# Kernel optimization log

Hardware: AMD Instinct MI355X
Metric: run time of the kernel (lower is better)

Reference implementation:

```python
import jax, jax.numpy as jnp
import numpy as np

B_, L_, D_, R_, N_ = 8, 1024, 512, 32, 16  # batch, seq(in_channels), dim(=dim_inner), dt_rank, d_state


def setup_inputs() -> dict:
    key = jax.random.key(0)
    ks = jax.random.split(key, 8)
    s = lambda k, shape, scale: jax.random.normal(k, shape, dtype=jnp.float32) * scale
    inv = D_ ** -0.5
    return {
        "x": jax.random.uniform(ks[0], (B_, L_, D_), dtype=jnp.float32),
        "W1": s(ks[1], (D_, D_), inv), "b1": jnp.zeros((D_,), jnp.float32),
        "W2": s(ks[2], (D_, D_), inv), "b2": jnp.zeros((D_,), jnp.float32),
        "Wout": s(ks[3], (D_, D_), inv), "bout": jnp.zeros((D_,), jnp.float32),
        "conv_w": s(ks[4], (L_, L_, 3), (3 * L_) ** -0.5),  # Conv1d(L_, L_, k=3) weight (O,I,W)
        "conv_b": jnp.zeros((L_,), jnp.float32),
        "W_dbc": s(ks[5], (R_ + 2 * N_, D_), inv),          # deltaBC projection (no bias)
        "W_dt": s(ks[6], (D_, R_), R_ ** -0.5),             # dt_proj weight
        "b_dt": jnp.zeros((D_,), jnp.float32),
        "A_log": jnp.log(jnp.tile(jnp.arange(1, N_ + 1, dtype=jnp.float32), (D_, 1))),  # (D, N)
        "Dp": jnp.ones((D_,), jnp.float32),
    }


def _silu(v):
    return v * jax.nn.sigmoid(v)


def _selective_scan(u, delta, A, Bm, Cm, Dp):
    # u, delta: (b, l, d); A: (d, n); Bm, Cm: (b, l, n); Dp: (d,)
    dA = jnp.exp(jnp.einsum('bld,dn->bldn', delta, A))          # (b,l,d,n)
    dBu = jnp.einsum('bld,bln,bld->bldn', delta, Bm, u)          # (b,l,d,n)

    def step(h, inp):
        dA_t, dBu_t, C_t = inp                                   # (b,d,n),(b,d,n),(b,n)
        h = dA_t * h + dBu_t
        return h, jnp.einsum('bdn,bn->bd', h, C_t)

    h0 = jnp.zeros((u.shape[0], u.shape[2], A.shape[1]), u.dtype)
    _, ys = jax.lax.scan(step, h0, (dA.transpose(1, 0, 2, 3), dBu.transpose(1, 0, 2, 3), Cm.transpose(1, 0, 2)))
    return ys.transpose(1, 0, 2) + u * Dp                        # (b,l,d)


def reference(x, W1, b1, W2, b2, Wout, bout, conv_w, conv_b, W_dbc, W_dt, b_dt, A_log, Dp):
    skip = x
    x1 = x @ W1.T + b1                                            # proj_one
    x2 = x @ W2.T + b2                                            # proj_two
    # Conv1d over channel axis = L_ (dim 1), spatial axis = D_ (dim 2)
    x1 = jax.lax.conv_general_dilated(x1, conv_w, window_strides=(1,), padding=((1, 1),),
                                      dimension_numbers=('NCW', 'OIW', 'NCW')) + conv_b[None, :, None]
    x1 = _silu(x1)
    # SSM (zeta-style): deltaBC -> split -> dt_proj -> softplus -> selective scan
    dbc = x1 @ W_dbc.T                                            # (b,l,R+2N)
    delta = jax.nn.softplus(dbc[..., :R_] @ W_dt.T + b_dt)        # (b,l,d)
    Bm, Cm = dbc[..., R_:R_ + N_], dbc[..., R_ + N_:]
    A = -jnp.exp(A_log)
    y = _selective_scan(x1, delta, A, Bm, Cm, Dp)
    out = y * _silu(x2) + skip
    return out @ Wout.T + bout
```

## Files before the change

kernel.cpp:

```cpp
#include <hip/hip_runtime.h>
#include <hip/hip_bf16.h>

typedef __hip_bfloat16 bf16;
typedef __bf16 bf16x8 __attribute__((ext_vector_type(8)));
typedef float f32x4 __attribute__((ext_vector_type(4)));

static_assert(sizeof(bf16) == 2, "bf16 must be 2 bytes");

#define NC 32
#define CH 32
#define X1TP_BSTRIDE (514L * 1024)

__device__ __forceinline__ float silu_f(float v) { return v / (1.0f + __expf(-v)); }

__device__ __forceinline__ void gload16(const bf16* g, bf16* l) {
  __builtin_amdgcn_global_load_lds((const __attribute__((address_space(1))) void*)g,
                                   (__attribute__((address_space(3))) void*)l,
                                   16, 0, 0);
}

template <int N> __device__ __forceinline__ void wait_vm() {
  static_assert(N == 0 || N == 4 || N == 6 || N == 8 || N == 12, "add case");
  if constexpr (N == 0)       asm volatile("s_waitcnt vmcnt(0)" ::: "memory");
  else if constexpr (N == 4)  asm volatile("s_waitcnt vmcnt(4)" ::: "memory");
  else if constexpr (N == 6)  asm volatile("s_waitcnt vmcnt(6)" ::: "memory");
  else if constexpr (N == 8)  asm volatile("s_waitcnt vmcnt(8)" ::: "memory");
  else if constexpr (N == 12) asm volatile("s_waitcnt vmcnt(12)" ::: "memory");
}

__global__ __launch_bounds__(256) void prep_all(
    const float* __restrict__ x, const float* __restrict__ W1,
    const float* __restrict__ W2, const float* __restrict__ Wout,
    const float* __restrict__ Wdbc, const float* __restrict__ convw,
    bf16* __restrict__ xb, bf16* __restrict__ w1b, bf16* __restrict__ w2b,
    bf16* __restrict__ woutb, bf16* __restrict__ wdbcb,
    bf16* __restrict__ cws, bf16* __restrict__ x1tp) {
  const int gid = blockIdx.x * 256 + threadIdx.x;
  auto cvt4 = [](const float* src, bf16* dst, long q) {
    float4 v = *reinterpret_cast<const float4*>(src + q * 4);
    ushort4 s;
    s.x = __builtin_bit_cast(unsigned short, __float2bfloat16(v.x));
    s.y = __builtin_bit_cast(unsigned short, __float2bfloat16(v.y));
    s.z = __builtin_bit_cast(unsigned short, __float2bfloat16(v.z));
    s.w = __builtin_bit_cast(unsigned short, __float2bfloat16(v.w));
    *reinterpret_cast<ushort4*>(dst + q * 4) = s;
  };
  if (gid < 1048576) {
    cvt4(x, xb, gid);
  } else if (gid < 1114112) {
    cvt4(W1, w1b, gid - 1048576);
  } else if (gid < 1179648) {
    cvt4(W2, w2b, gid - 1114112);
  } else if (gid < 1245184) {
    cvt4(Wout, woutb, gid - 1179648);
  } else if (gid < 1253376) {
    cvt4(Wdbc, wdbcb, gid - 1245184);
  } else if (gid < 2301952) {
    long idx = gid - 1253376;
    int o = (int)(idx >> 10), i = (int)(idx & 1023);
    float a = convw[idx * 3], b = convw[idx * 3 + 1], c = convw[idx * 3 + 2];
    cws[(long)o * 3072 + i]        = __float2bfloat16(a);
    cws[(long)o * 3072 + 1024 + i] = __float2bfloat16(b);
    cws[(long)o * 3072 + 2048 + i] = __float2bfloat16(c);
  } else {
    int e = gid - 2301952;
    int b = e >> 11, rem = e & 2047;
    int r = rem >> 10, ii = rem & 1023;
    x1tp[(long)b * X1TP_BSTRIDE + (long)r * (513 * 1024) + ii] = __float2bfloat16(0.f);
  }
}

template <int EPI, int BM, int BN, int CONVB, int NBUF>
__device__ __forceinline__ void gemm_body(const bf16* __restrict__ A,
                                          const bf16* __restrict__ Bw,
                                          const float* __restrict__ bias,
                                          float* __restrict__ outf,
                                          bf16* __restrict__ outb,
                                          int M, int N, int K, int lda, int ldb,
                                          long sAz, long sBz, long sOz,
                                          int bx, int by, int z,
                                          bf16* As, bf16* Bs) {
  constexpr int BK = 64;
  constexpr int MI = BM / 32, WNF = BN / 32;
  constexpr int APW = BM / 32, BPW = BN / 32;
  constexpr int IPW = APW + BPW;

  const int tid = threadIdx.x;
  const int w = tid >> 6, l = tid & 63;
  const int wm = w >> 1, wn = w & 1;
  const int m0 = bx * BM, n0 = by * BN;
  const bf16* Ab = A + (long)z * sAz + (long)m0 * lda;
  const bf16* Bb = Bw + (long)z * sBz;

  const int lrow = l >> 3;
  const int lcol = (((l & 7) ^ (l >> 3)) << 3);

  auto stage = [&](int buf, int k0) {
#pragma unroll
    for (int j = 0; j < APW; ++j) {
      int iss = w * APW + j;
      int row = iss * 8 + lrow;
      gload16(Ab + (long)row * lda + k0 + lcol, &As[buf * BM * 64 + iss * 512]);
    }
#pragma unroll
    for (int j = 0; j < BPW; ++j) {
      int iss = w * BPW + j;
      int row = iss * 8 + lrow;
      const bf16* src;
      if (CONVB) src = Bb + (long)(n0 + row + (k0 >> 10)) * 1024 + (k0 & 1023) + lcol;
      else       src = Bb + (long)(n0 + row) * ldb + k0 + lcol;
      gload16(src, &Bs[buf * BN * 64 + iss * 512]);
    }
  };

  f32x4 acc[MI][WNF] = {};
  const int nt = K / BK;
  const int lr = l & 15;
  const int lko = (l >> 4) * 8;
  const int xorm = (lr & 7) << 3;

#pragma unroll
  for (int s = 0; s < NBUF - 1; ++s) stage(s, s * BK);
  for (int t = 0; t < nt; ++t) {
    const int cur = t % NBUF;
    if (t + NBUF - 1 < nt) {
      stage((t + NBUF - 1) % NBUF, (t + NBUF - 1) * BK);
      wait_vm<(NBUF - 1) * IPW>();
    } else {
      wait_vm<0>();
    }
    __builtin_amdgcn_s_barrier();
    __builtin_amdgcn_sched_barrier(0);
#pragma unroll
    for (int kk = 0; kk < 2; ++kk) {
      const int col = (lko + kk * 32) ^ xorm;
      bf16x8 af[MI], bfg[WNF];
#pragma unroll
      for (int mi = 0; mi < MI; ++mi)
        af[mi] = *reinterpret_cast<const bf16x8*>(
            &As[cur * BM * 64 + (wm * (BM / 2) + mi * 16 + lr) * 64 + col]);
#pragma unroll
      for (int ni = 0; ni < WNF; ++ni)
        bfg[ni] = *reinterpret_cast<const bf16x8*>(
            &Bs[cur * BN * 64 + (wn * (BN / 2) + ni * 16 + lr) * 64 + col]);
#pragma unroll
      for (int mi = 0; mi < MI; ++mi)
#pragma unroll
        for (int ni = 0; ni < WNF; ++ni)
          acc[mi][ni] = __builtin_amdgcn_mfma_f32_16x16x32_bf16(af[mi], bfg[ni], acc[mi][ni], 0, 0, 0);
    }
    __builtin_amdgcn_sched_barrier(0);
    __builtin_amdgcn_s_barrier();
  }

  const int lq = l >> 4;
#pragma unroll
  for (int mi = 0; mi < MI; ++mi) {
#pragma unroll
    for (int ni = 0; ni < WNF; ++ni) {
#pragma unroll
      for (int j = 0; j < 4; ++j) {
        int m = m0 + wm * (BM / 2) + mi * 16 + lq * 4 + j;
        int n = n0 + wn * (BN / 2) + ni * 16 + lr;
        float v = acc[mi][ni][j];
        if (EPI == 2) {
          v += bias[m];
          (outb + (long)z * sOz)[(long)m * N + n] = __float2bfloat16(silu_f(v));
        } else if (EPI == 3) {
          outf[(long)m * N + n] = v;
        } else if (EPI == 4) {
          v += bias[n];
          outf[(long)m * N + n] = v;
        } else if (EPI == 5) {
          v += bias[m];
          int b = n >> 10, li = n & 1023;
          outb[(long)b * X1TP_BSTRIDE + (long)(m + 1) * 1024 + li] = __float2bfloat16(v);
        } else {
          v += bias[n];
          outb[(long)m * N + n] = __float2bfloat16(silu_f(v));
        }
      }
    }
  }
}

template <int EPI, int BM, int BN, int CONVB, int NBUF, int GX, int GY>
__global__ __launch_bounds__(256) void gemm_nt(const bf16* __restrict__ A,
                                               const bf16* __restrict__ Bw,
                                               const float* __restrict__ bias,
                                               float* __restrict__ outf,
                                               bf16* __restrict__ outb,
                                               int M, int N, int K, int lda, int ldb,
                                               long sAz, long sBz, long sOz) {
  __shared__ __align__(16) bf16 As[NBUF * BM * 64];
  __shared__ __align__(16) bf16 Bs[NBUF * BN * 64];
  const int bid = (blockIdx.x & 7) * ((int)gridDim.x >> 3) + (blockIdx.x >> 3);
  const int by = bid % GY;
  const int bx = (bid / GY) % GX;
  const int z  = bid / (GX * GY);
  gemm_body<EPI, BM, BN, CONVB, NBUF>(A, Bw, bias, outf, outb, M, N, K, lda, ldb,
                                      sAz, sBz, sOz, bx, by, z, As, Bs);
}

__global__ __launch_bounds__(256) void gemm_dual(
    const bf16* __restrict__ w1b, const bf16* __restrict__ xb1,
    const float* __restrict__ b1, bf16* __restrict__ x1tp,
    const bf16* __restrict__ xb2, const bf16* __restrict__ w2b,
    const float* __restrict__ b2, bf16* __restrict__ x2g) {
  __shared__ __align__(16) bf16 As[2 * 128 * 64];
  __shared__ __align__(16) bf16 Bs[2 * 128 * 64];
  int bid = (blockIdx.x & 7) * 64 + (blockIdx.x >> 3);
  if (bid < 256) {
    int by = bid & 63, bx = bid >> 6;
    gemm_body<5, 128, 128, 0, 2>(w1b, xb1, b1, nullptr, x1tp, 512, 8192, 512, 512, 512,
                                 0, 0, 0, bx, by, 0, As, Bs);
  } else {
    bid -= 256;
    int by = bid & 3, bx = bid >> 2;
    gemm_body<6, 128, 128, 0, 2>(xb2, w2b, b2, nullptr, x2g, 8192, 512, 512, 512, 512,
                                 0, 0, 0, bx, by, 0, As, Bs);
  }
}

__global__ __launch_bounds__(256) void delta_kernel(const float* __restrict__ dbc,
                                                    const float* __restrict__ W_dt,
                                                    const float* __restrict__ b_dt,
                                                    float* __restrict__ delta) {
  const int tid = threadIdx.x;
  const int d = blockIdx.x * 256 + tid;
  const int r0 = blockIdx.y * 8;
  __shared__ float sD[8][32];
  {
    int tt = tid >> 5, j = tid & 31;
    sD[tt][j] = dbc[(long)(r0 + tt) * 64 + j];
  }
  __syncthreads();
  float wdt[32];
#pragma unroll
  for (int r = 0; r < 32; r += 4) {
    float4 v = *reinterpret_cast<const float4*>(&W_dt[(long)d * 32 + r]);
    wdt[r] = v.x; wdt[r + 1] = v.y; wdt[r + 2] = v.z; wdt[r + 3] = v.w;
  }
  const float bd = b_dt[d];
#pragma unroll
  for (int tt = 0; tt < 8; ++tt) {
    float a = bd;
#pragma unroll
    for (int r = 0; r < 32; ++r) a = fmaf(sD[tt][r], wdt[r], a);
    delta[(long)(r0 + tt) * 512 + d] = fmaxf(a, 0.f) + log1pf(__expf(-fabsf(a)));
  }
}

__global__ __launch_bounds__(256) void scan_p1(const bf16* __restrict__ u_bf,
                                               const float* __restrict__ dbc,
                                               const float* __restrict__ delta,
                                               const float* __restrict__ A_log,
                                               float* __restrict__ P,
                                               float* __restrict__ Q) {
  const int tid = threadIdx.x;
  const int nh = tid & 1;
  const int d = blockIdx.x * 128 + (tid >> 1);
  const int c = blockIdx.y, b = blockIdx.z;
  __shared__ float sB[CH][16];
  for (int i = tid; i < CH * 16; i += 256) {
    int tt = i >> 4, j = i & 15;
    sB[tt][j] = dbc[((long)b * 1024 + c * CH + tt) * 64 + 32 + j];
  }
  __syncthreads();
  float Adn[8];
#pragma unroll
  for (int n = 0; n < 8; ++n) Adn[n] = -__expf(A_log[d * 16 + nh * 8 + n]);
  float p[8], q[8];
#pragma unroll
  for (int n = 0; n < 8; ++n) { p[n] = 1.f; q[n] = 0.f; }
  const long rowb = (long)b * 1024 + c * CH;
  for (int tt = 0; tt < CH; ++tt) {
    long off = (rowb + tt) * 512 + d;
    float dv = delta[off];
    float uv = __bfloat162float(u_bf[off]);
    float s = dv * uv;
#pragma unroll
    for (int n = 0; n < 8; ++n) {
      float dA = __expf(dv * Adn[n]);
      p[n] *= dA;
      q[n] = fmaf(dA, q[n], s * sB[tt][nh * 8 + n]);
    }
  }
  float* Pp = P + ((long)b * NC + c) * 8192 + (long)d * 16 + nh * 8;
  float* Qp = Q + ((long)b * NC + c) * 8192 + (long)d * 16 + nh * 8;
  *reinterpret_cast<float4*>(Pp)     = make_float4(p[0], p[1], p[2], p[3]);
  *reinterpret_cast<float4*>(Pp + 4) = make_float4(p[4], p[5], p[6], p[7]);
  *reinterpret_cast<float4*>(Qp)     = make_float4(q[0], q[1], q[2], q[3]);
  *reinterpret_cast<float4*>(Qp + 4) = make_float4(q[4], q[5], q[6], q[7]);
}

__global__ __launch_bounds__(256) void scan_p2(const float* __restrict__ P,
                                               const float* __restrict__ Q,
                                               float* __restrict__ Hin) {
  const int dn = blockIdx.x * 256 + threadIdx.x;
  const int b = blockIdx.y;
  float h = 0.f;
#pragma unroll 4
  for (int c = 0; c < NC; ++c) {
    long idx = ((long)b * NC + c) * 8192 + dn;
    Hin[idx] = h;
    h = fmaf(P[idx], h, Q[idx]);
  }
}

__global__ __launch_bounds__(256) void scan_p3(const bf16* __restrict__ u_bf,
                                               const float* __restrict__ dbc,
                                               const float* __restrict__ delta,
                                               const float* __restrict__ A_log,
                                               const float* __restrict__ Dp,
                                               const bf16* __restrict__ x2g,
                                               const bf16* __restrict__ xres,
                                               const float* __restrict__ Hin,
                                               bf16* __restrict__ zb) {
  const int tid = threadIdx.x;
  const int nh = tid & 1;
  const int d = blockIdx.x * 128 + (tid >> 1);
  const int c = blockIdx.y, b = blockIdx.z;
  __shared__ float sBC[CH][32];
  for (int i = tid; i < CH * 32; i += 256) {
    int tt = i >> 5, j = i & 31;
    sBC[tt][j] = dbc[((long)b * 1024 + c * CH + tt) * 64 + 32 + j];
  }
  __syncthreads();
  float Adn[8];
#pragma unroll
  for (int n = 0; n < 8; ++n) Adn[n] = -__expf(A_log[d * 16 + nh * 8 + n]);
  float h[8];
  const float* Hp = Hin + ((long)b * NC + c) * 8192 + (long)d * 16 + nh * 8;
  {
    float4 v0 = *reinterpret_cast<const float4*>(Hp);
    float4 v1 = *reinterpret_cast<const float4*>(Hp + 4);
    h[0] = v0.x; h[1] = v0.y; h[2] = v0.z; h[3] = v0.w;
    h[4] = v1.x; h[5] = v1.y; h[6] = v1.z; h[7] = v1.w;
  }
  const float Dpv = Dp[d];
  const long rowb = (long)b * 1024 + c * CH;
  for (int tt = 0; tt < CH; ++tt) {
    long off = (rowb + tt) * 512 + d;
    float dv = delta[off];
    float uv = __bfloat162float(u_bf[off]);
    float s = dv * uv;
    float y = nh ? 0.f : uv * Dpv;
#pragma unroll
    for (int n = 0; n < 8; ++n) {
      float dA = __expf(dv * Adn[n]);
      h[n] = fmaf(dA, h[n], s * sBC[tt][nh * 8 + n]);
      y = fmaf(h[n], sBC[tt][16 + nh * 8 + n], y);
    }
    y += __shfl_xor(y, 1);
    if (nh == 0) {
      float gate = __bfloat162float(x2g[off]);
      float xv = __bfloat162float(xres[off]);
      zb[off] = __float2bfloat16(fmaf(y, gate, xv));
    }
  }
}

extern "C" void kernel_launch(void* const* d_in, const int* in_sizes, int n_in,
                              void* d_out, int out_size, void* d_ws, size_t ws_size,
                              hipStream_t stream) {
  (void)in_sizes; (void)n_in; (void)out_size; (void)ws_size;
  const float* x    = (const float*)d_in[0];
  const float* W1   = (const float*)d_in[1];
  const float* b1   = (const float*)d_in[2];
  const float* W2   = (const float*)d_in[3];
  const float* b2   = (const float*)d_in[4];
  const float* Wout = (const float*)d_in[5];
  const float* bout = (const float*)d_in[6];
  const float* convw = (const float*)d_in[7];
  const float* convb = (const float*)d_in[8];
  const float* Wdbc = (const float*)d_in[9];
  const float* Wdt  = (const float*)d_in[10];
  const float* bdt  = (const float*)d_in[11];
  const float* Alog = (const float*)d_in[12];
  const float* Dp   = (const float*)d_in[13];
  float* out = (float*)d_out;

  char* ws = (char*)d_ws;
  size_t off = 0;
  auto alloc = [&](size_t bytes) { void* p = ws + off; off += (bytes + 255) & ~(size_t)255; return p; };
  bf16* xb     = (bf16*)alloc(8192L * 512 * 2);
  bf16* w1b    = (bf16*)alloc(512L * 512 * 2);
  bf16* w2b    = (bf16*)alloc(512L * 512 * 2);
  bf16* woutb  = (bf16*)alloc(512L * 512 * 2);
  bf16* wdbcb  = (bf16*)alloc(64L * 512 * 2);
  bf16* cws    = (bf16*)alloc(1024L * 3072 * 2);
  bf16* x1tp   = (bf16*)alloc(8L * X1TP_BSTRIDE * 2);
  bf16* x2g    = (bf16*)alloc(8192L * 512 * 2);
  bf16* x1s    = (bf16*)alloc(8192L * 512 * 2);
  float* dbc   = (float*)alloc(8192L * 64 * 4);
  float* delta = (float*)alloc(8192L * 512 * 4);
  float* P     = (float*)alloc(8L * NC * 8192 * 4);
  float* Q     = (float*)alloc(8L * NC * 8192 * 4);
  float* Hin   = (float*)alloc(8L * NC * 8192 * 4);
  bf16* zb = xb;

  prep_all<<<9056, 256, 0, stream>>>(x, W1, W2, Wout, Wdbc, convw,
                                     xb, w1b, w2b, woutb, wdbcb, cws, x1tp);
  gemm_dual<<<512, 256, 0, stream>>>(w1b, xb, b1, x1tp, xb, w2b, b2, x2g);
  gemm_nt<2, 64, 128, 1, 3, 16, 4><<<512, 256, 0, stream>>>(
      cws, x1tp, convb, nullptr, x1s, 1024, 512, 3072, 3072, 0,
      0, X1TP_BSTRIDE, 1024L * 512);
  gemm_nt<3, 64, 64, 0, 3, 128, 1><<<128, 256, 0, stream>>>(
      x1s, wdbcb, nullptr, dbc, nullptr, 8192, 64, 512, 512, 512, 0, 0, 0);
  delta_kernel<<<dim3(2, 1024), 256, 0, stream>>>(dbc, Wdt, bdt, delta);
  scan_p1<<<dim3(4, NC, 8), 256, 0, stream>>>(x1s, dbc, delta, Alog, P, Q);
  scan_p2<<<dim3(32, 8, 1), 256, 0, stream>>>(P, Q, Hin);
  scan_p3<<<dim3(4, NC, 8), 256, 0, stream>>>(x1s, dbc, delta, Alog, Dp, x2g, xb, Hin, zb);
  gemm_nt<4, 64, 128, 0, 3, 128, 4><<<512, 256, 0, stream>>>(
      zb, woutb, bout, out, nullptr, 8192, 512, 512, 512, 512, 0, 0, 0);
}
```

Measured before the change: 162.8 us.

## Fuse delta projection into scan pass one and store scan intermediates in fp16

Removes the standalone delta kernel and computes the dt projection plus softplus inside scan_p1, splitting the 32-term dot product across the two lanes that share a channel and combining them with a shuffle. Delta, the chunk decay products P, the chunk states Q and the carried state Hin are now stored as fp16 instead of fp32. This saves one launch and halves the traffic for these intermediates. The risk is precision: chunk decay products can underflow in fp16, and the state carried between chunks loses accuracy.

```diff
diff --git a/kernel.cpp b/kernel.cpp
--- a/kernel.cpp
+++ b/kernel.cpp
@@ -1,5 +1,6 @@
 #include <hip/hip_runtime.h>
 #include <hip/hip_bf16.h>
+#include <hip/hip_fp16.h>
 
 typedef __hip_bfloat16 bf16;
 typedef __bf16 bf16x8 __attribute__((ext_vector_type(8)));
@@ -222,51 +223,31 @@
   }
 }
 
-__global__ __launch_bounds__(256) void delta_kernel(const float* __restrict__ dbc,
-                                                    const float* __restrict__ W_dt,
-                                                    const float* __restrict__ b_dt,
-                                                    float* __restrict__ delta) {
-  const int tid = threadIdx.x;
-  const int d = blockIdx.x * 256 + tid;
-  const int r0 = blockIdx.y * 8;
-  __shared__ float sD[8][32];
-  {
-    int tt = tid >> 5, j = tid & 31;
-    sD[tt][j] = dbc[(long)(r0 + tt) * 64 + j];
-  }
-  __syncthreads();
-  float wdt[32];
-#pragma unroll
-  for (int r = 0; r < 32; r += 4) {
-    float4 v = *reinterpret_cast<const float4*>(&W_dt[(long)d * 32 + r]);
-    wdt[r] = v.x; wdt[r + 1] = v.y; wdt[r + 2] = v.z; wdt[r + 3] = v.w;
-  }
-  const float bd = b_dt[d];
-#pragma unroll
-  for (int tt = 0; tt < 8; ++tt) {
-    float a = bd;
-#pragma unroll
-    for (int r = 0; r < 32; ++r) a = fmaf(sD[tt][r], wdt[r], a);
-    delta[(long)(r0 + tt) * 512 + d] = fmaxf(a, 0.f) + log1pf(__expf(-fabsf(a)));
-  }
-}
-
 __global__ __launch_bounds__(256) void scan_p1(const bf16* __restrict__ u_bf,
                                                const float* __restrict__ dbc,
-                                               const float* __restrict__ delta,
+                                               const float* __restrict__ W_dt,
+                                               const float* __restrict__ b_dt,
                                                const float* __restrict__ A_log,
-                                               float* __restrict__ P,
-                                               float* __restrict__ Q) {
+                                               __half* __restrict__ delta_h,
+                                               __half* __restrict__ P,
+                                               __half* __restrict__ Q) {
   const int tid = threadIdx.x;
   const int nh = tid & 1;
   const int d = blockIdx.x * 128 + (tid >> 1);
   const int c = blockIdx.y, b = blockIdx.z;
-  __shared__ float sB[CH][16];
-  for (int i = tid; i < CH * 16; i += 256) {
-    int tt = i >> 4, j = i & 15;
-    sB[tt][j] = dbc[((long)b * 1024 + c * CH + tt) * 64 + 32 + j];
+  __shared__ float sD[CH][48];
+  for (int i = tid; i < CH * 48; i += 256) {
+    int tt = i / 48, j = i % 48;
+    sD[tt][j] = dbc[((long)b * 1024 + c * CH + tt) * 64 + j];
   }
   __syncthreads();
+  float wdt[16];
+#pragma unroll
+  for (int r = 0; r < 16; r += 4) {
+    float4 v = *reinterpret_cast<const float4*>(&W_dt[(long)d * 32 + nh * 16 + r]);
+    wdt[r] = v.x; wdt[r + 1] = v.y; wdt[r + 2] = v.z; wdt[r + 3] = v.w;
+  }
+  const float bd = b_dt[d];
   float Adn[8];
 #pragma unroll
   for (int n = 0; n < 8; ++n) Adn[n] = -__expf(A_log[d * 16 + nh * 8 + n]);
@@ -276,46 +257,53 @@
   const long rowb = (long)b * 1024 + c * CH;
   for (int tt = 0; tt < CH; ++tt) {
     long off = (rowb + tt) * 512 + d;
-    float dv = delta[off];
+    float ah = 0.f;
+#pragma unroll
+    for (int r = 0; r < 16; ++r) ah = fmaf(sD[tt][nh * 16 + r], wdt[r], ah);
+    ah += __shfl_xor(ah, 1);
+    float a = bd + ah;
+    float dv = fmaxf(a, 0.f) + log1pf(__expf(-fabsf(a)));
+    if (nh == 0) delta_h[off] = __float2half(dv);
     float uv = __bfloat162float(u_bf[off]);
     float s = dv * uv;
 #pragma unroll
     for (int n = 0; n < 8; ++n) {
       float dA = __expf(dv * Adn[n]);
       p[n] *= dA;
-      q[n] = fmaf(dA, q[n], s * sB[tt][nh * 8 + n]);
-    }
-  }
-  float* Pp = P + ((long)b * NC + c) * 8192 + (long)d * 16 + nh * 8;
-  float* Qp = Q + ((long)b * NC + c) * 8192 + (long)d * 16 + nh * 8;
-  *reinterpret_cast<float4*>(Pp)     = make_float4(p[0], p[1], p[2], p[3]);
-  *reinterpret_cast<float4*>(Pp + 4) = make_float4(p[4], p[5], p[6], p[7]);
-  *reinterpret_cast<float4*>(Qp)     = make_float4(q[0], q[1], q[2], q[3]);
-  *reinterpret_cast<float4*>(Qp + 4) = make_float4(q[4], q[5], q[6], q[7]);
-}
-
-__global__ __launch_bounds__(256) void scan_p2(const float* __restrict__ P,
-                                               const float* __restrict__ Q,
-                                               float* __restrict__ Hin) {
+      q[n] = fmaf(dA, q[n], s * sD[tt][32 + nh * 8 + n]);
+    }
+  }
+  __half* Pp = P + ((long)b * NC + c) * 8192 + (long)d * 16 + nh * 8;
+  __half* Qp = Q + ((long)b * NC + c) * 8192 + (long)d * 16 + nh * 8;
+  __half tp[8], tq[8];
+#pragma unroll
+  for (int n = 0; n < 8; ++n) { tp[n] = __float2half(p[n]); tq[n] = __float2half(q[n]); }
+  *reinterpret_cast<uint4*>(Pp) = *reinterpret_cast<uint4*>(tp);
+  *reinterpret_cast<uint4*>(Qp) = *reinterpret_cast<uint4*>(tq);
+}
+
+__global__ __launch_bounds__(256) void scan_p2(const __half* __restrict__ P,
+                                               const __half* __restrict__ Q,
+                                               __half* __restrict__ Hin) {
   const int dn = blockIdx.x * 256 + threadIdx.x;
   const int b = blockIdx.y;
   float h = 0.f;
 #pragma unroll 4
   for (int c = 0; c < NC; ++c) {
     long idx = ((long)b * NC + c) * 8192 + dn;
-    Hin[idx] = h;
-    h = fmaf(P[idx], h, Q[idx]);
+    Hin[idx] = __float2half(h);
+    h = fmaf(__half2float(P[idx]), h, __half2float(Q[idx]));
   }
 }
 
 __global__ __launch_bounds__(256) void scan_p3(const bf16* __restrict__ u_bf,
                                                const float* __restrict__ dbc,
-                                               const float* __restrict__ delta,
+                                               const __half* __restrict__ delta_h,
                                                const float* __restrict__ A_log,
                                                const float* __restrict__ Dp,
                                                const bf16* __restrict__ x2g,
                                                const bf16* __restrict__ xres,
-                                               const float* __restrict__ Hin,
+                                               const __half* __restrict__ Hin,
                                                bf16* __restrict__ zb) {
   const int tid = threadIdx.x;
   const int nh = tid & 1;
@@ -331,18 +319,18 @@
 #pragma unroll
   for (int n = 0; n < 8; ++n) Adn[n] = -__expf(A_log[d * 16 + nh * 8 + n]);
   float h[8];
-  const float* Hp = Hin + ((long)b * NC + c) * 8192 + (long)d * 16 + nh * 8;
   {
-    float4 v0 = *reinterpret_cast<const float4*>(Hp);
-    float4 v1 = *reinterpret_cast<const float4*>(Hp + 4);
-    h[0] = v0.x; h[1] = v0.y; h[2] = v0.z; h[3] = v0.w;
-    h[4] = v1.x; h[5] = v1.y; h[6] = v1.z; h[7] = v1.w;
+    const __half* Hp = Hin + ((long)b * NC + c) * 8192 + (long)d * 16 + nh * 8;
+    __half th[8];
+    *reinterpret_cast<uint4*>(th) = *reinterpret_cast<const uint4*>(Hp);
+#pragma unroll
+    for (int n = 0; n < 8; ++n) h[n] = __half2float(th[n]);
   }
   const float Dpv = Dp[d];
   const long rowb = (long)b * 1024 + c * CH;
   for (int tt = 0; tt < CH; ++tt) {
     long off = (rowb + tt) * 512 + d;
-    float dv = delta[off];
+    float dv = __half2float(delta_h[off]);
     float uv = __bfloat162float(u_bf[off]);
     float s = dv * uv;
     float y = nh ? 0.f : uv * Dpv;
@@ -384,20 +372,20 @@
   char* ws = (char*)d_ws;
   size_t off = 0;
   auto alloc = [&](size_t bytes) { void* p = ws + off; off += (bytes + 255) & ~(size_t)255; return p; };
-  bf16* xb     = (bf16*)alloc(8192L * 512 * 2);
-  bf16* w1b    = (bf16*)alloc(512L * 512 * 2);
-  bf16* w2b    = (bf16*)alloc(512L * 512 * 2);
-  bf16* woutb  = (bf16*)alloc(512L * 512 * 2);
-  bf16* wdbcb  = (bf16*)alloc(64L * 512 * 2);
-  bf16* cws    = (bf16*)alloc(1024L * 3072 * 2);
-  bf16* x1tp   = (bf16*)alloc(8L * X1TP_BSTRIDE * 2);
-  bf16* x2g    = (bf16*)alloc(8192L * 512 * 2);
-  bf16* x1s    = (bf16*)alloc(8192L * 512 * 2);
-  float* dbc   = (float*)alloc(8192L * 64 * 4);
-  float* delta = (float*)alloc(8192L * 512 * 4);
-  float* P     = (float*)alloc(8L * NC * 8192 * 4);
-  float* Q     = (float*)alloc(8L * NC * 8192 * 4);
-  float* Hin   = (float*)alloc(8L * NC * 8192 * 4);
+  bf16* xb      = (bf16*)alloc(8192L * 512 * 2);
+  bf16* w1b     = (bf16*)alloc(512L * 512 * 2);
+  bf16* w2b     = (bf16*)alloc(512L * 512 * 2);
+  bf16* woutb   = (bf16*)alloc(512L * 512 * 2);
+  bf16* wdbcb   = (bf16*)alloc(64L * 512 * 2);
+  bf16* cws     = (bf16*)alloc(1024L * 3072 * 2);
+  bf16* x1tp    = (bf16*)alloc(8L * X1TP_BSTRIDE * 2);
+  bf16* x2g     = (bf16*)alloc(8192L * 512 * 2);
+  bf16* x1s     = (bf16*)alloc(8192L * 512 * 2);
+  float* dbc    = (float*)alloc(8192L * 64 * 4);
+  __half* delta = (__half*)alloc(8192L * 512 * 2);
+  __half* P     = (__half*)alloc(8L * NC * 8192 * 2);
+  __half* Q     = (__half*)alloc(8L * NC * 8192 * 2);
+  __half* Hin   = (__half*)alloc(8L * NC * 8192 * 2);
   bf16* zb = xb;
 
   prep_all<<<9056, 256, 0, stream>>>(x, W1, W2, Wout, Wdbc, convw,
@@ -408,8 +396,7 @@
       0, X1TP_BSTRIDE, 1024L * 512);
   gemm_nt<3, 64, 64, 0, 3, 128, 1><<<128, 256, 0, stream>>>(
       x1s, wdbcb, nullptr, dbc, nullptr, 8192, 64, 512, 512, 512, 0, 0, 0);
-  delta_kernel<<<dim3(2, 1024), 256, 0, stream>>>(dbc, Wdt, bdt, delta);
-  scan_p1<<<dim3(4, NC, 8), 256, 0, stream>>>(x1s, dbc, delta, Alog, P, Q);
+  scan_p1<<<dim3(4, NC, 8), 256, 0, stream>>>(x1s, dbc, Wdt, bdt, Alog, delta, P, Q);
   scan_p2<<<dim3(32, 8, 1), 256, 0, stream>>>(P, Q, Hin);
   scan_p3<<<dim3(4, NC, 8), 256, 0, stream>>>(x1s, dbc, delta, Alog, Dp, x2g, xb, Hin, zb);
   gemm_nt<4, 64, 128, 0, 3, 128, 4><<<512, 256, 0, stream>>>(
```

Result: slower. 169.6 us (+4.2%).
